# Kernel tuning notes

Hardware: AMD Instinct MI355X
Metric: run time of the kernel (lower is better)

Reference implementation:

```python
import jax, jax.numpy as jnp
import numpy as np

B, S, T = 1024, 512, 48


def setup_inputs() -> dict:
    key = jax.random.key(0)
    k1, k2, k3, k4, k5 = jax.random.split(key, 5)
    feats = jax.random.normal(k1, (B, S, T), dtype=jnp.float32)
    tags = jax.random.randint(k2, (B, S), 0, T)
    mask = jnp.ones((B, S), dtype=bool)
    transitions = jax.random.normal(k3, (T, T), dtype=jnp.float32)
    start_transitions = jax.random.normal(k4, (T,), dtype=jnp.float32)
    stop_transitions = jax.random.normal(k5, (T,), dtype=jnp.float32)
    return dict(feats=feats, tags=tags, mask=mask, transitions=transitions,
                start_transitions=start_transitions, stop_transitions=stop_transitions)


def _crf_nll(feats, transitions, start_transitions, stop_transitions, tags, mask):
    # ----- forward algorithm (log partition) -----
    fv0 = start_transitions + feats[:, 0]                      # (B, T)

    def step(fv, xs):
        feat_t, mask_t = xs                                    # (B, T), (B,)
        # transitions[next, cur]: fv over cur axis (last)
        nxt = jax.nn.logsumexp(fv[:, None, :] + transitions[None, :, :]
                               + feat_t[:, :, None], axis=-1)  # (B, T)
        fv = jnp.where(mask_t[:, None], nxt, fv)
        return fv, None

    feats_t = jnp.swapaxes(feats, 0, 1)                        # (S, B, T)
    fv, _ = jax.lax.scan(step, fv0, (feats_t[1:], mask.T[1:]))
    log_z = jax.nn.logsumexp(fv + stop_transitions, axis=-1)   # (B,)

    # ----- gold path score -----
    emit = jnp.take_along_axis(feats, tags[..., None], axis=2)[..., 0]   # (B, S)
    trans = transitions[tags[:, 1:], tags[:, :-1]]                       # (B, S-1)
    gold = emit[:, 0] + start_transitions[tags[:, 0]]
    gold = gold + jnp.sum(jnp.where(mask[:, 1:], trans + emit[:, 1:], 0.0), axis=1)
    last_idx = mask.astype(jnp.int32).sum(axis=1) - 1                    # (B,)
    last_tag = jnp.take_along_axis(tags, last_idx[:, None], axis=1)[:, 0]
    gold = gold + stop_transitions[last_tag]

    return jnp.mean(log_z - gold)


def reference(feats, tags, mask, transitions, start_transitions, stop_transitions):
    return _crf_nll(feats, transitions, start_transitions, stop_transitions, tags, mask)
```

## Files before the change

### kernel.cpp

```cpp
#include <hip/hip_runtime.h>
#include <hip/hip_bf16.h>
#include <math.h>

#define BB 1024
#define SS 512
#define MID 256
#define TT 48
#define BPW 16
#define FWB 16
#define BWB 16

typedef __attribute__((ext_vector_type(8))) short short8;
typedef __attribute__((ext_vector_type(4))) float f32x4;
typedef __attribute__((ext_vector_type(4))) unsigned u32x4;
typedef __attribute__((ext_vector_type(2))) unsigned u32x2;

__device__ __forceinline__ unsigned short f2bf_u(float x) {
    return __builtin_bit_cast(unsigned short, __float2bfloat16(x));
}
__device__ __forceinline__ unsigned pk_bf16(float lo, float hi) {
    return (unsigned)f2bf_u(lo) | ((unsigned)f2bf_u(hi) << 16);
}
__device__ __forceinline__ short f2bf(float x) { return (short)f2bf_u(x); }

template<int CTRL>
__device__ __forceinline__ float dpp_f(float v) {
    int r = __builtin_amdgcn_update_dpp(0, __builtin_bit_cast(int, v),
                                        CTRL, 0xF, 0xF, true);
    return __builtin_bit_cast(float, r);
}
__device__ __forceinline__ float waveSum(float v) {
    v += dpp_f<0x111>(v);
    v += dpp_f<0x112>(v);
    v += dpp_f<0x114>(v);
    v += dpp_f<0x118>(v);
    v += dpp_f<0x142>(v);
    v += dpp_f<0x143>(v);
    return __builtin_bit_cast(float,
        __builtin_amdgcn_readlane(__builtin_bit_cast(int, v), 63));
}

__global__ __launch_bounds__(256, 1) void crf_main(
    const float* __restrict__ feats, const int* __restrict__ tags,
    const float* __restrict__ trans, const float* __restrict__ startT,
    const float* __restrict__ stopT,
    float* __restrict__ qf, float* __restrict__ cf,
    float* __restrict__ qb, float* __restrict__ cb,
    float* __restrict__ gold)
{
    const int wv = threadIdx.x >> 6;
    const int lane = threadIdx.x & 63;

    if (blockIdx.x < FWB + BWB) {
        const bool isF = blockIdx.x < FWB;
        __shared__ unsigned Qb_[4][16][28];
        __shared__ int ptab[4][16];
        const int c = lane & 15;
        const int g = lane >> 4;
        const int bi = isF ? blockIdx.x : (blockIdx.x - FWB);
        const int b0 = (bi * 4 + wv) * BPW;
        const float* fb = feats + (size_t)(b0 + c) * SS * TT;
        unsigned (*Q)[28] = Qb_[wv];

        int pic;
        {
            if (lane < 16) ptab[wv][lane] = lane;
            const short one = f2bf(1.0f);
            short8 PA, PB;
            #pragma unroll
            for (int j = 0; j < 8; j++) {
                PA[j] = (g == 0) ? one : (short)0;
                PB[j] = f2bf((float)c);
            }
            f32x4 z = {0.f, 0.f, 0.f, 0.f};
            f32x4 PD = __builtin_amdgcn_mfma_f32_16x16x32_bf16(PA, PB, z, 0, 0, 0);
            int piv = (int)(PD[0] * 0.125f + 0.5f);
            piv = piv < 0 ? 0 : (piv > 15 ? 15 : piv);
            if (g == 0) ptab[wv][piv] = c;
            pic = ptab[wv][c];
            pic = pic < 0 ? 0 : (pic > 15 ? 15 : pic);
        }

        short8 Afr[3][2];
        #pragma unroll
        for (int r = 0; r < 3; r++)
            #pragma unroll
            for (int s = 0; s < 2; s++) {
                short8 v;
                #pragma unroll
                for (int j = 0; j < 8; j++) {
                    int k = 8 * g + j + 32 * s;
                    int row = 16 * r + c;
                    float e = (k < TT)
                        ? __expf(isF ? trans[row * TT + k] : trans[k * TT + row])
                        : 0.0f;
                    v[j] = f2bf(e);
                }
                Afr[r][s] = v;
            }

        f32x4 prods[3];
        float c_acc = 0.0f;
        float pend_is = 1.0f, pend_lg = 0.0f;
        f32x4 rA[3], rB[3], Ecur[3];

        #define PUBLISH_READ() do {                                          \
            _Pragma("unroll")                                                \
            for (int r = 0; r < 3; r++) {                                    \
                u32x2 w = { pk_bf16(prods[r][0], prods[r][1]),               \
                            pk_bf16(prods[r][2], prods[r][3]) };             \
                *(u32x2*)(&Q[c][8 * r + 2 * g]) = w;                         \
            }                                                                \
            const unsigned* src = &Q[pic][0];                                \
            B0 = __builtin_bit_cast(short8, *(const u32x4*)(src + 4 * g));   \
            if (g < 2)                                                       \
                B1 = __builtin_bit_cast(short8, *(const u32x4*)(src + 16 + 4 * g)); \
            else { u32x4 zz = {0u,0u,0u,0u}; B1 = __builtin_bit_cast(short8, zz); } \
        } while (0)

        #define MEASURE() do {                                               \
            float mx = 0.0f;                                                 \
            _Pragma("unroll")                                                \
            for (int r = 0; r < 3; r++)                                      \
                _Pragma("unroll")                                            \
                for (int j = 0; j < 4; j++) {                                \
                    prods[r][j] = fminf(prods[r][j], 1e30f);                 \
                    mx = fmaxf(mx, prods[r][j]);                             \
                }                                                            \
            mx = fmaxf(mx, __shfl_xor(mx, 16));                              \
            mx = fmaxf(mx, __shfl_xor(mx, 32));                              \
            mx = fminf(fmaxf(mx, 1e-30f), 3e37f);                            \
            pend_is = __builtin_amdgcn_rcpf(mx);                             \
            pend_lg = __logf(mx);                                            \
        } while (0)

        #define FOLD() do {                                                  \
            c_acc += pend_lg;                                                \
            _Pragma("unroll")                                                \
            for (int r = 0; r < 3; r++) Ecur[r] *= pend_is;                  \
        } while (0)

        short8 B0, B1;

        if (isF) {
            {
                f32x4 fv[3];
                #pragma unroll
                for (int r = 0; r < 3; r++) {
                    f32x4 st = *(const f32x4*)(startT + 16 * r + 4 * g);
                    f32x4 f0 = *(const f32x4*)(fb + 16 * r + 4 * g);
                    fv[r] = st + f0;
                }
                float mx = fv[0][0];
                #pragma unroll
                for (int r = 0; r < 3; r++)
                    #pragma unroll
                    for (int j = 0; j < 4; j++) mx = fmaxf(mx, fv[r][j]);
                mx = fmaxf(mx, __shfl_xor(mx, 16));
                mx = fmaxf(mx, __shfl_xor(mx, 32));
                c_acc = mx;
                #pragma unroll
                for (int r = 0; r < 3; r++)
                    #pragma unroll
                    for (int j = 0; j < 4; j++)
                        prods[r][j] = __expf(fv[r][j] - mx);
            }
            PUBLISH_READ();
            #pragma unroll
            for (int r = 0; r < 3; r++) {
                f32x4 r1 = *(const f32x4*)(fb + (size_t)1 * TT + 16 * r + 4 * g);
                rA[r] = *(const f32x4*)(fb + (size_t)2 * TT + 16 * r + 4 * g);
                rB[r] = *(const f32x4*)(fb + (size_t)3 * TT + 16 * r + 4 * g);
                f32x4 e;
                #pragma unroll
                for (int j = 0; j < 4; j++) e[j] = __expf(r1[j]);
                Ecur[r] = e;
            }

            #pragma unroll 4
            for (int t = 1; t <= MID; t++) {
                int tl = (t + 3 <= MID) ? t + 3 : MID;
                f32x4 rN[3];
                #pragma unroll
                for (int r = 0; r < 3; r++)
                    rN[r] = *(const f32x4*)(fb + (size_t)tl * TT + 16 * r + 4 * g);

                f32x4 D[3];
                #pragma unroll
                for (int r = 0; r < 3; r++) {
                    f32x4 z = {0.f, 0.f, 0.f, 0.f};
                    z = __builtin_amdgcn_mfma_f32_16x16x32_bf16(Afr[r][0], B0, z, 0, 0, 0);
                    z = __builtin_amdgcn_mfma_f32_16x16x32_bf16(Afr[r][1], B1, z, 0, 0, 0);
                    D[r] = z;
                }
                if ((t & 3) == 1) FOLD();
                #pragma unroll
                for (int r = 0; r < 3; r++) prods[r] = D[r] * Ecur[r];
                if ((t & 3) == 0) MEASURE();
                PUBLISH_READ();
                #pragma unroll
                for (int r = 0; r < 3; r++) {
                    f32x4 e;
                    #pragma unroll
                    for (int j = 0; j < 4; j++) e[j] = __expf(rA[r][j]);
                    Ecur[r] = e;
                    rA[r] = rB[r];
                    rB[r] = rN[r];
                }
            }
            #pragma unroll
            for (int r = 0; r < 3; r++)
                *(f32x4*)(qf + (size_t)(b0 + c) * TT + 16 * r + 4 * g) = prods[r];
            if (g == 0) cf[b0 + c] = c_acc;
        } else {
            #pragma unroll
            for (int r = 0; r < 3; r++) {
                f32x4 sp = *(const f32x4*)(stopT + 16 * r + 4 * g);
                #pragma unroll
                for (int j = 0; j < 4; j++) prods[r][j] = __expf(sp[j]);
            }
            #pragma unroll
            for (int r = 0; r < 3; r++) {
                f32x4 r1 = *(const f32x4*)(fb + (size_t)(SS - 1) * TT + 16 * r + 4 * g);
                rA[r] = *(const f32x4*)(fb + (size_t)(SS - 2) * TT + 16 * r + 4 * g);
                rB[r] = *(const f32x4*)(fb + (size_t)(SS - 3) * TT + 16 * r + 4 * g);
                f32x4 e;
                #pragma unroll
                for (int j = 0; j < 4; j++) e[j] = __expf(r1[j]);
                Ecur[r] = e;
            }

            #pragma unroll 4
            for (int t = SS - 1; t >= MID + 1; t--) {
                int tl = (t - 3 >= 0) ? t - 3 : 0;
                f32x4 rN[3];
                #pragma unroll
                for (int r = 0; r < 3; r++)
                    rN[r] = *(const f32x4*)(fb + (size_t)tl * TT + 16 * r + 4 * g);

                if ((t & 3) == 3) FOLD();
                #pragma unroll
                for (int r = 0; r < 3; r++) prods[r] = prods[r] * Ecur[r];
                PUBLISH_READ();
                f32x4 D[3];
                #pragma unroll
                for (int r = 0; r < 3; r++) {
                    f32x4 z = {0.f, 0.f, 0.f, 0.f};
                    z = __builtin_amdgcn_mfma_f32_16x16x32_bf16(Afr[r][0], B0, z, 0, 0, 0);
                    z = __builtin_amdgcn_mfma_f32_16x16x32_bf16(Afr[r][1], B1, z, 0, 0, 0);
                    D[r] = z;
                }
                #pragma unroll
                for (int r = 0; r < 3; r++) prods[r] = D[r];
                if ((t & 3) == 0) MEASURE();
                #pragma unroll
                for (int r = 0; r < 3; r++) {
                    f32x4 e;
                    #pragma unroll
                    for (int j = 0; j < 4; j++) e[j] = __expf(rA[r][j]);
                    Ecur[r] = e;
                    rA[r] = rB[r];
                    rB[r] = rN[r];
                }
            }
            #pragma unroll
            for (int r = 0; r < 3; r++)
                *(f32x4*)(qb + (size_t)(b0 + c) * TT + 16 * r + 4 * g) = prods[r];
            if (g == 0) cb[b0 + c] = c_acc;
        }
        #undef PUBLISH_READ
        #undef MEASURE
        #undef FOLD
    } else {
        const int b = (blockIdx.x - FWB - BWB) * 4 + wv;
        const int* tg = tags + b * SS;
        const float* fbg = feats + (size_t)b * SS * TT;
        float acc = 0.0f;
        for (int t = lane; t < SS; t += 64) {
            int cur = tg[t];
            if (t == 0) {
                acc += fbg[cur] + startT[cur];
            } else {
                int prev = tg[t - 1];
                acc += fbg[t * TT + cur] + trans[cur * TT + prev];
            }
        }
        float tot = waveSum(acc);
        if (lane == 0) gold[b] = tot + stopT[tg[SS - 1]];
    }
}

__global__ __launch_bounds__(256) void crf_final(
    const float* __restrict__ qf, const float* __restrict__ cf,
    const float* __restrict__ qb, const float* __restrict__ cb,
    const float* __restrict__ gold, float* __restrict__ out)
{
    __shared__ double sh[256];
    int t = threadIdx.x;
    double s = 0.0;
    for (int b = t * 4; b < t * 4 + 4; b++) {
        float acc = 0.0f;
        for (int j = 0; j < TT; j++)
            acc += qf[(size_t)b * TT + j] * qb[(size_t)b * TT + j];
        acc = fminf(fmaxf(acc, 1e-35f), 3e37f);
        float lz = cf[b] + cb[b] + __logf(acc);
        s += (double)lz - (double)gold[b];
    }
    sh[t] = s;
    __syncthreads();
    for (int ofs = 128; ofs > 0; ofs >>= 1) {
        if (t < ofs) sh[t] += sh[t + ofs];
        __syncthreads();
    }
    if (t == 0) out[0] = (float)(sh[0] / (double)BB);
}

extern "C" void kernel_launch(void* const* d_in, const int* in_sizes, int n_in,
                              void* d_out, int out_size, void* d_ws, size_t ws_size,
                              hipStream_t stream)
{
    const float* feats  = (const float*)d_in[0];
    const int*   tags   = (const int*)d_in[1];
    const float* trans  = (const float*)d_in[3];
    const float* startT = (const float*)d_in[4];
    const float* stopT  = (const float*)d_in[5];

    float* gold = (float*)d_ws;
    float* qf   = gold + BB;
    float* cf   = qf + BB * TT;
    float* qb   = cf + BB;
    float* cb   = qb + BB * TT;

    crf_main<<<FWB + BWB + 256, 256, 0, stream>>>(
        feats, tags, trans, startT, stopT, qf, cf, qb, cb, gold);
    crf_final<<<1, 256, 0, stream>>>(qf, cf, qb, cb, gold, (float*)d_out);
}
```

Before: 123.0 us.

## Precompute exp(feats) as bf16 in a parallel prepass before the sequential CRF scan

Adds a bandwidth-parallel prepass kernel that exponentiates all emission scores and stores them as bf16 in workspace, computing the gold path scores in the same launch. The sequential forward/backward kernel then loads half as many bytes per step and only bit-unpacks them, with no exp on the recurrence path. The sequential kernel now uses 8 waves per 512-thread block and prefetches four steps ahead instead of three. The cost is an extra full pass over feats plus a large workspace write, and emissions lose precision when rounded to bf16. A fallback path without the prepass is kept for when the workspace is too small.

```diff
diff --git a/kernel.cpp b/kernel.cpp
--- a/kernel.cpp
+++ b/kernel.cpp
@@ -1,14 +1,13 @@
 #include <hip/hip_runtime.h>
 #include <hip/hip_bf16.h>
 #include <math.h>
+#include <type_traits>
 
 #define BB 1024
 #define SS 512
 #define MID 256
 #define TT 48
-#define BPW 16
-#define FWB 16
-#define BWB 16
+#define CONVB 1024
 
 typedef __attribute__((ext_vector_type(8))) short short8;
 typedef __attribute__((ext_vector_type(4))) float f32x4;
@@ -22,6 +21,15 @@
     return (unsigned)f2bf_u(lo) | ((unsigned)f2bf_u(hi) << 16);
 }
 __device__ __forceinline__ short f2bf(float x) { return (short)f2bf_u(x); }
+
+__device__ __forceinline__ f32x4 unpk4(u32x2 w) {
+    f32x4 e;
+    e[0] = __builtin_bit_cast(float, w[0] << 16);
+    e[1] = __builtin_bit_cast(float, w[0] & 0xffff0000u);
+    e[2] = __builtin_bit_cast(float, w[1] << 16);
+    e[3] = __builtin_bit_cast(float, w[1] & 0xffff0000u);
+    return e;
+}
 
 template<int CTRL>
 __device__ __forceinline__ float dpp_f(float v) {
@@ -40,254 +48,294 @@
         __builtin_amdgcn_readlane(__builtin_bit_cast(int, v), 63));
 }
 
-__global__ __launch_bounds__(256, 1) void crf_main(
-    const float* __restrict__ feats, const int* __restrict__ tags,
-    const float* __restrict__ trans, const float* __restrict__ startT,
-    const float* __restrict__ stopT,
+__device__ __forceinline__ void gold_wave(
+    int b, int lane, const float* feats, const int* tags, const float* trans,
+    const float* startT, const float* stopT, float* gold)
+{
+    const int* tg = tags + b * SS;
+    const float* fbg = feats + (size_t)b * SS * TT;
+    float acc = 0.0f;
+    for (int t = lane; t < SS; t += 64) {
+        int cur = tg[t];
+        if (t == 0) {
+            acc += fbg[cur] + startT[cur];
+        } else {
+            int prev = tg[t - 1];
+            acc += fbg[t * TT + cur] + trans[cur * TT + prev];
+        }
+    }
+    float tot = waveSum(acc);
+    if (lane == 0) gold[b] = tot + stopT[tg[SS - 1]];
+}
+
+__global__ __launch_bounds__(256) void crf_prepass(
+    const float* __restrict__ feats, unsigned short* __restrict__ G,
+    const int* __restrict__ tags, const float* __restrict__ trans,
+    const float* __restrict__ startT, const float* __restrict__ stopT,
+    float* __restrict__ gold)
+{
+    if (blockIdx.x < CONVB) {
+        const size_t NB4 = (size_t)BB * SS * TT / 4;
+        const float4* src = (const float4*)feats;
+        ushort4* dst = (ushort4*)G;
+        for (size_t i = (size_t)blockIdx.x * 256 + threadIdx.x; i < NB4;
+             i += (size_t)CONVB * 256) {
+            float4 v = src[i];
+            ushort4 o;
+            o.x = f2bf_u(__expf(v.x));
+            o.y = f2bf_u(__expf(v.y));
+            o.z = f2bf_u(__expf(v.z));
+            o.w = f2bf_u(__expf(v.w));
+            dst[i] = o;
+        }
+    } else {
+        const int wv = threadIdx.x >> 6;
+        const int lane = threadIdx.x & 63;
+        gold_wave((blockIdx.x - CONVB) * 4 + wv, lane,
+                  feats, tags, trans, startT, stopT, gold);
+    }
+}
+
+template<bool PRE>
+__global__ __launch_bounds__(512, 2) void crf_seq(
+    const float* __restrict__ feats, const unsigned short* __restrict__ G,
+    const int* __restrict__ tags, const float* __restrict__ trans,
+    const float* __restrict__ startT, const float* __restrict__ stopT,
     float* __restrict__ qf, float* __restrict__ cf,
     float* __restrict__ qb, float* __restrict__ cb,
     float* __restrict__ gold)
 {
-    const int wv = threadIdx.x >> 6;
+    const int w = threadIdx.x >> 6;
     const int lane = threadIdx.x & 63;
 
-    if (blockIdx.x < FWB + BWB) {
-        const bool isF = blockIdx.x < FWB;
-        __shared__ unsigned Qb_[4][16][28];
-        __shared__ int ptab[4][16];
-        const int c = lane & 15;
-        const int g = lane >> 4;
-        const int bi = isF ? blockIdx.x : (blockIdx.x - FWB);
-        const int b0 = (bi * 4 + wv) * BPW;
-        const float* fb = feats + (size_t)(b0 + c) * SS * TT;
-        unsigned (*Q)[28] = Qb_[wv];
-
-        int pic;
+    if (blockIdx.x >= 16) {
+        gold_wave((blockIdx.x - 16) * 8 + w, lane,
+                  feats, tags, trans, startT, stopT, gold);
+        return;
+    }
+
+    const bool isF = blockIdx.x < 8;
+    __shared__ unsigned Q_[8][16][28];
+    __shared__ int ptab[8][16];
+    const int c = lane & 15;
+    const int g = lane >> 4;
+    const int bi = (isF ? blockIdx.x : blockIdx.x - 8) * 8 + w;
+    const int b0 = bi * 16;
+    const float* fb = feats + (size_t)(b0 + c) * SS * TT;
+    const unsigned short* gb = G + (size_t)(b0 + c) * SS * TT;
+    unsigned (*Q)[28] = Q_[w];
+
+    int pic;
+    {
+        if (lane < 16) ptab[w][lane] = lane;
+        const short one = f2bf(1.0f);
+        short8 PA, PB;
+        #pragma unroll
+        for (int j = 0; j < 8; j++) {
+            PA[j] = (g == 0) ? one : (short)0;
+            PB[j] = f2bf((float)c);
+        }
+        f32x4 z = {0.f, 0.f, 0.f, 0.f};
+        f32x4 PD = __builtin_amdgcn_mfma_f32_16x16x32_bf16(PA, PB, z, 0, 0, 0);
+        int piv = (int)(PD[0] * 0.125f + 0.5f);
+        piv = piv < 0 ? 0 : (piv > 15 ? 15 : piv);
+        if (g == 0) ptab[w][piv] = c;
+        pic = ptab[w][c];
+        pic = pic < 0 ? 0 : (pic > 15 ? 15 : pic);
+    }
+
+    short8 Afr[3][2];
+    #pragma unroll
+    for (int r = 0; r < 3; r++)
+        #pragma unroll
+        for (int s = 0; s < 2; s++) {
+            short8 v;
+            #pragma unroll
+            for (int j = 0; j < 8; j++) {
+                int k = 8 * g + j + 32 * s;
+                int row = 16 * r + c;
+                float e = (k < TT)
+                    ? __expf(isF ? trans[row * TT + k] : trans[k * TT + row])
+                    : 0.0f;
+                v[j] = f2bf(e);
+            }
+            Afr[r][s] = v;
+        }
+
+    auto LD = [&](int t, int r) {
+        if constexpr (PRE)
+            return *(const u32x2*)(gb + (size_t)t * TT + 16 * r + 4 * g);
+        else
+            return *(const f32x4*)(fb + (size_t)t * TT + 16 * r + 4 * g);
+    };
+    auto PROM = [&](auto v) -> f32x4 {
+        if constexpr (PRE) {
+            return unpk4(v);
+        } else {
+            f32x4 e;
+            #pragma unroll
+            for (int j = 0; j < 4; j++) e[j] = __expf(v[j]);
+            return e;
+        }
+    };
+    using LT = decltype(LD(0, 0));
+
+    f32x4 prods[3];
+    float c_acc = 0.0f;
+    float pend_is = 1.0f, pend_lg = 0.0f;
+    LT rA[3], rB[3], rC[3];
+    f32x4 Ecur[3];
+    short8 B0, B1;
+
+    #define PUBLISH_READ() do {                                          \
+        _Pragma("unroll")                                                \
+        for (int r = 0; r < 3; r++) {                                    \
+            u32x2 wd = { pk_bf16(prods[r][0], prods[r][1]),              \
+                         pk_bf16(prods[r][2], prods[r][3]) };            \
+            *(u32x2*)(&Q[c][8 * r + 2 * g]) = wd;                        \
+        }                                                                \
+        const unsigned* src = &Q[pic][0];                                \
+        B0 = __builtin_bit_cast(short8, *(const u32x4*)(src + 4 * g));   \
+        if (g < 2)                                                       \
+            B1 = __builtin_bit_cast(short8, *(const u32x4*)(src + 16 + 4 * g)); \
+        else { u32x4 zz = {0u,0u,0u,0u}; B1 = __builtin_bit_cast(short8, zz); } \
+    } while (0)
+
+    #define MEASURE() do {                                               \
+        float mx = 0.0f;                                                 \
+        _Pragma("unroll")                                                \
+        for (int r = 0; r < 3; r++)                                      \
+            _Pragma("unroll")                                            \
+            for (int j = 0; j < 4; j++) {                                \
+                prods[r][j] = fminf(prods[r][j], 1e30f);                 \
+                mx = fmaxf(mx, prods[r][j]);                             \
+            }                                                            \
+        mx = fmaxf(mx, __shfl_xor(mx, 16));                              \
+        mx = fmaxf(mx, __shfl_xor(mx, 32));                              \
+        mx = fminf(fmaxf(mx, 1e-30f), 3e37f);                            \
+        pend_is = __builtin_amdgcn_rcpf(mx);                             \
+        pend_lg = __logf(mx);                                            \
+    } while (0)
+
+    #define FOLD() do {                                                  \
+        c_acc += pend_lg;                                                \
+        _Pragma("unroll")                                                \
+        for (int r = 0; r < 3; r++) Ecur[r] *= pend_is;                  \
+    } while (0)
+
+    if (isF) {
         {
-            if (lane < 16) ptab[wv][lane] = lane;
-            const short one = f2bf(1.0f);
-            short8 PA, PB;
-            #pragma unroll
-            for (int j = 0; j < 8; j++) {
-                PA[j] = (g == 0) ? one : (short)0;
-                PB[j] = f2bf((float)c);
-            }
-            f32x4 z = {0.f, 0.f, 0.f, 0.f};
-            f32x4 PD = __builtin_amdgcn_mfma_f32_16x16x32_bf16(PA, PB, z, 0, 0, 0);
-            int piv = (int)(PD[0] * 0.125f + 0.5f);
-            piv = piv < 0 ? 0 : (piv > 15 ? 15 : piv);
-            if (g == 0) ptab[wv][piv] = c;
-            pic = ptab[wv][c];
-            pic = pic < 0 ? 0 : (pic > 15 ? 15 : pic);
-        }
-
-        short8 Afr[3][2];
+            f32x4 fv[3];
+            #pragma unroll
+            for (int r = 0; r < 3; r++) {
+                f32x4 st = *(const f32x4*)(startT + 16 * r + 4 * g);
+                f32x4 f0 = *(const f32x4*)(fb + 16 * r + 4 * g);
+                fv[r] = st + f0;
+            }
+            float mx = fv[0][0];
+            #pragma unroll
+            for (int r = 0; r < 3; r++)
+                #pragma unroll
+                for (int j = 0; j < 4; j++) mx = fmaxf(mx, fv[r][j]);
+            mx = fmaxf(mx, __shfl_xor(mx, 16));
+            mx = fmaxf(mx, __shfl_xor(mx, 32));
+            c_acc = mx;
+            #pragma unroll
+            for (int r = 0; r < 3; r++)
+                #pragma unroll
+                for (int j = 0; j < 4; j++)
+                    prods[r][j] = __expf(fv[r][j] - mx);
+        }
+        PUBLISH_READ();
+        #pragma unroll
+        for (int r = 0; r < 3; r++) {
+            Ecur[r] = PROM(LD(1, r));
+            rA[r] = LD(2, r);
+            rB[r] = LD(3, r);
+            rC[r] = LD(4, r);
+        }
+
+        #pragma unroll 4
+        for (int t = 1; t <= MID; t++) {
+            int tl = (t + 4 <= MID) ? t + 4 : MID;
+            LT rN[3];
+            #pragma unroll
+            for (int r = 0; r < 3; r++) rN[r] = LD(tl, r);
+
+            f32x4 D[3];
+            #pragma unroll
+            for (int r = 0; r < 3; r++) {
+                f32x4 z = {0.f, 0.f, 0.f, 0.f};
+                z = __builtin_amdgcn_mfma_f32_16x16x32_bf16(Afr[r][0], B0, z, 0, 0, 0);
+                z = __builtin_amdgcn_mfma_f32_16x16x32_bf16(Afr[r][1], B1, z, 0, 0, 0);
+                D[r] = z;
+            }
+            if ((t & 3) == 1) FOLD();
+            #pragma unroll
+            for (int r = 0; r < 3; r++) prods[r] = D[r] * Ecur[r];
+            if ((t & 3) == 0) MEASURE();
+            PUBLISH_READ();
+            #pragma unroll
+            for (int r = 0; r < 3; r++) {
+                Ecur[r] = PROM(rA[r]);
+                rA[r] = rB[r]; rB[r] = rC[r]; rC[r] = rN[r];
+            }
+        }
         #pragma unroll
         for (int r = 0; r < 3; r++)
-            #pragma unroll
-            for (int s = 0; s < 2; s++) {
-                short8 v;
-                #pragma unroll
-                for (int j = 0; j < 8; j++) {
-                    int k = 8 * g + j + 32 * s;
-                    int row = 16 * r + c;
-                    float e = (k < TT)
-                        ? __expf(isF ? trans[row * TT + k] : trans[k * TT + row])
-                        : 0.0f;
-                    v[j] = f2bf(e);
-                }
-                Afr[r][s] = v;
-            }
-
-        f32x4 prods[3];
-        float c_acc = 0.0f;
-        float pend_is = 1.0f, pend_lg = 0.0f;
-        f32x4 rA[3], rB[3], Ecur[3];
-
-        #define PUBLISH_READ() do {                                          \
-            _Pragma("unroll")                                                \
-            for (int r = 0; r < 3; r++) {                                    \
-                u32x2 w = { pk_bf16(prods[r][0], prods[r][1]),               \
-                            pk_bf16(prods[r][2], prods[r][3]) };             \
-                *(u32x2*)(&Q[c][8 * r + 2 * g]) = w;                         \
-            }                                                                \
-            const unsigned* src = &Q[pic][0];                                \
-            B0 = __builtin_bit_cast(short8, *(const u32x4*)(src + 4 * g));   \
-            if (g < 2)                                                       \
-                B1 = __builtin_bit_cast(short8, *(const u32x4*)(src + 16 + 4 * g)); \
-            else { u32x4 zz = {0u,0u,0u,0u}; B1 = __builtin_bit_cast(short8, zz); } \
-        } while (0)
-
-        #define MEASURE() do {                                               \
-            float mx = 0.0f;                                                 \
-            _Pragma("unroll")                                                \
-            for (int r = 0; r < 3; r++)                                      \
-                _Pragma("unroll")                                            \
-                for (int j = 0; j < 4; j++) {                                \
-                    prods[r][j] = fminf(prods[r][j], 1e30f);                 \
-                    mx = fmaxf(mx, prods[r][j]);                             \
-                }                                                            \
-            mx = fmaxf(mx, __shfl_xor(mx, 16));                              \
-            mx = fmaxf(mx, __shfl_xor(mx, 32));                              \
-            mx = fminf(fmaxf(mx, 1e-30f), 3e37f);                            \
-            pend_is = __builtin_amdgcn_rcpf(mx);                             \
-            pend_lg = __logf(mx);                                            \
-        } while (0)
-
-        #define FOLD() do {                                                  \
-            c_acc += pend_lg;                                                \
-            _Pragma("unroll")                                                \
-            for (int r = 0; r < 3; r++) Ecur[r] *= pend_is;                  \
-        } while (0)
-
-        short8 B0, B1;
-
-        if (isF) {
-            {
-                f32x4 fv[3];
-                #pragma unroll
-                for (int r = 0; r < 3; r++) {
-                    f32x4 st = *(const f32x4*)(startT + 16 * r + 4 * g);
-                    f32x4 f0 = *(const f32x4*)(fb + 16 * r + 4 * g);
-                    fv[r] = st + f0;
-                }
-                float mx = fv[0][0];
-                #pragma unroll
-                for (int r = 0; r < 3; r++)
-                    #pragma unroll
-                    for (int j = 0; j < 4; j++) mx = fmaxf(mx, fv[r][j]);
-                mx = fmaxf(mx, __shfl_xor(mx, 16));
-                mx = fmaxf(mx, __shfl_xor(mx, 32));
-                c_acc = mx;
-                #pragma unroll
-                for (int r = 0; r < 3; r++)
-                    #pragma unroll
-                    for (int j = 0; j < 4; j++)
-                        prods[r][j] = __expf(fv[r][j] - mx);
-            }
+            *(f32x4*)(qf + (size_t)(b0 + c) * TT + 16 * r + 4 * g) = prods[r];
+        if (g == 0) cf[b0 + c] = c_acc;
+    } else {
+        #pragma unroll
+        for (int r = 0; r < 3; r++) {
+            f32x4 sp = *(const f32x4*)(stopT + 16 * r + 4 * g);
+            #pragma unroll
+            for (int j = 0; j < 4; j++) prods[r][j] = __expf(sp[j]);
+        }
+        #pragma unroll
+        for (int r = 0; r < 3; r++) {
+            Ecur[r] = PROM(LD(SS - 1, r));
+            rA[r] = LD(SS - 2, r);
+            rB[r] = LD(SS - 3, r);
+            rC[r] = LD(SS - 4, r);
+        }
+
+        #pragma unroll 4
+        for (int t = SS - 1; t >= MID + 1; t--) {
+            int tl = (t - 4 >= 0) ? t - 4 : 0;
+            LT rN[3];
+            #pragma unroll
+            for (int r = 0; r < 3; r++) rN[r] = LD(tl, r);
+
+            if ((t & 3) == 3) FOLD();
+            #pragma unroll
+            for (int r = 0; r < 3; r++) prods[r] = prods[r] * Ecur[r];
             PUBLISH_READ();
-            #pragma unroll
-            for (int r = 0; r < 3; r++) {
-                f32x4 r1 = *(const f32x4*)(fb + (size_t)1 * TT + 16 * r + 4 * g);
-                rA[r] = *(const f32x4*)(fb + (size_t)2 * TT + 16 * r + 4 * g);
-                rB[r] = *(const f32x4*)(fb + (size_t)3 * TT + 16 * r + 4 * g);
-                f32x4 e;
-                #pragma unroll
-                for (int j = 0; j < 4; j++) e[j] = __expf(r1[j]);
-                Ecur[r] = e;
-            }
-
-            #pragma unroll 4
-            for (int t = 1; t <= MID; t++) {
-                int tl = (t + 3 <= MID) ? t + 3 : MID;
-                f32x4 rN[3];
-                #pragma unroll
-                for (int r = 0; r < 3; r++)
-                    rN[r] = *(const f32x4*)(fb + (size_t)tl * TT + 16 * r + 4 * g);
-
-                f32x4 D[3];
-                #pragma unroll
-                for (int r = 0; r < 3; r++) {
-                    f32x4 z = {0.f, 0.f, 0.f, 0.f};
-                    z = __builtin_amdgcn_mfma_f32_16x16x32_bf16(Afr[r][0], B0, z, 0, 0, 0);
-                    z = __builtin_amdgcn_mfma_f32_16x16x32_bf16(Afr[r][1], B1, z, 0, 0, 0);
-                    D[r] = z;
-                }
-                if ((t & 3) == 1) FOLD();
-                #pragma unroll
-                for (int r = 0; r < 3; r++) prods[r] = D[r] * Ecur[r];
-                if ((t & 3) == 0) MEASURE();
-                PUBLISH_READ();
-                #pragma unroll
-                for (int r = 0; r < 3; r++) {
-                    f32x4 e;
-                    #pragma unroll
-                    for (int j = 0; j < 4; j++) e[j] = __expf(rA[r][j]);
-                    Ecur[r] = e;
-                    rA[r] = rB[r];
-                    rB[r] = rN[r];
-                }
-            }
-            #pragma unroll
-            for (int r = 0; r < 3; r++)
-                *(f32x4*)(qf + (size_t)(b0 + c) * TT + 16 * r + 4 * g) = prods[r];
-            if (g == 0) cf[b0 + c] = c_acc;
-        } else {
-            #pragma unroll
-            for (int r = 0; r < 3; r++) {
-                f32x4 sp = *(const f32x4*)(stopT + 16 * r + 4 * g);
-                #pragma unroll
-                for (int j = 0; j < 4; j++) prods[r][j] = __expf(sp[j]);
-            }
-            #pragma unroll
-            for (int r = 0; r < 3; r++) {
-                f32x4 r1 = *(const f32x4*)(fb + (size_t)(SS - 1) * TT + 16 * r + 4 * g);
-                rA[r] = *(const f32x4*)(fb + (size_t)(SS - 2) * TT + 16 * r + 4 * g);
-                rB[r] = *(const f32x4*)(fb + (size_t)(SS - 3) * TT + 16 * r + 4 * g);
-                f32x4 e;
-                #pragma unroll
-                for (int j = 0; j < 4; j++) e[j] = __expf(r1[j]);
-                Ecur[r] = e;
-            }
-
-            #pragma unroll 4
-            for (int t = SS - 1; t >= MID + 1; t--) {
-                int tl = (t - 3 >= 0) ? t - 3 : 0;
-                f32x4 rN[3];
-                #pragma unroll
-                for (int r = 0; r < 3; r++)
-                    rN[r] = *(const f32x4*)(fb + (size_t)tl * TT + 16 * r + 4 * g);
-
-                if ((t & 3) == 3) FOLD();
-                #pragma unroll
-                for (int r = 0; r < 3; r++) prods[r] = prods[r] * Ecur[r];
-                PUBLISH_READ();
-                f32x4 D[3];
-                #pragma unroll
-                for (int r = 0; r < 3; r++) {
-                    f32x4 z = {0.f, 0.f, 0.f, 0.f};
-                    z = __builtin_amdgcn_mfma_f32_16x16x32_bf16(Afr[r][0], B0, z, 0, 0, 0);
-                    z = __builtin_amdgcn_mfma_f32_16x16x32_bf16(Afr[r][1], B1, z, 0, 0, 0);
-                    D[r] = z;
-                }
-                #pragma unroll
-                for (int r = 0; r < 3; r++) prods[r] = D[r];
-                if ((t & 3) == 0) MEASURE();
-                #pragma unroll
-                for (int r = 0; r < 3; r++) {
-                    f32x4 e;
-                    #pragma unroll
-                    for (int j = 0; j < 4; j++) e[j] = __expf(rA[r][j]);
-                    Ecur[r] = e;
-                    rA[r] = rB[r];
-                    rB[r] = rN[r];
-                }
-            }
-            #pragma unroll
-            for (int r = 0; r < 3; r++)
-                *(f32x4*)(qb + (size_t)(b0 + c) * TT + 16 * r + 4 * g) = prods[r];
-            if (g == 0) cb[b0 + c] = c_acc;
-        }
-        #undef PUBLISH_READ
-        #undef MEASURE
-        #undef FOLD
-    } else {
-        const int b = (blockIdx.x - FWB - BWB) * 4 + wv;
-        const int* tg = tags + b * SS;
-        const float* fbg = feats + (size_t)b * SS * TT;
-        float acc = 0.0f;
-        for (int t = lane; t < SS; t += 64) {
-            int cur = tg[t];
-            if (t == 0) {
-                acc += fbg[cur] + startT[cur];
-            } else {
-                int prev = tg[t - 1];
-                acc += fbg[t * TT + cur] + trans[cur * TT + prev];
-            }
-        }
-        float tot = waveSum(acc);
-        if (lane == 0) gold[b] = tot + stopT[tg[SS - 1]];
-    }
+            f32x4 D[3];
+            #pragma unroll
+            for (int r = 0; r < 3; r++) {
+                f32x4 z = {0.f, 0.f, 0.f, 0.f};
+                z = __builtin_amdgcn_mfma_f32_16x16x32_bf16(Afr[r][0], B0, z, 0, 0, 0);
+                z = __builtin_amdgcn_mfma_f32_16x16x32_bf16(Afr[r][1], B1, z, 0, 0, 0);
+                D[r] = z;
+            }
+            #pragma unroll
+            for (int r = 0; r < 3; r++) prods[r] = D[r];
+            if ((t & 3) == 0) MEASURE();
+            #pragma unroll
+            for (int r = 0; r < 3; r++) {
+                Ecur[r] = PROM(rA[r]);
+                rA[r] = rB[r]; rB[r] = rC[r]; rC[r] = rN[r];
+            }
+        }
+        #pragma unroll
+        for (int r = 0; r < 3; r++)
+            *(f32x4*)(qb + (size_t)(b0 + c) * TT + 16 * r + 4 * g) = prods[r];
+        if (g == 0) cb[b0 + c] = c_acc;
+    }
+    #undef PUBLISH_READ
+    #undef MEASURE
+    #undef FOLD
 }
 
 __global__ __launch_bounds__(256) void crf_final(
@@ -325,13 +373,26 @@
     const float* startT = (const float*)d_in[4];
     const float* stopT  = (const float*)d_in[5];
 
-    float* gold = (float*)d_ws;
-    float* qf   = gold + BB;
-    float* cf   = qf + BB * TT;
-    float* qb   = cf + BB;
-    float* cb   = qb + BB * TT;
-
-    crf_main<<<FWB + BWB + 256, 256, 0, stream>>>(
-        feats, tags, trans, startT, stopT, qf, cf, qb, cb, gold);
+    const size_t GBYTES = (size_t)BB * SS * TT * 2;
+    const size_t TAILF  = (size_t)BB * (1 + TT + 1 + TT + 1);
+    const bool pre = ws_size >= GBYTES + TAILF * 4 + 64;
+
+    char* p = (char*)d_ws;
+    unsigned short* G = (unsigned short*)p;
+    float* gold = (float*)(p + (pre ? GBYTES : 0));
+    float* qf = gold + BB;
+    float* cf = qf + BB * TT;
+    float* qb = cf + BB;
+    float* cb = qb + BB * TT;
+
+    if (pre) {
+        crf_prepass<<<CONVB + 256, 256, 0, stream>>>(
+            feats, G, tags, trans, startT, stopT, gold);
+        crf_seq<true><<<16, 512, 0, stream>>>(
+            feats, G, tags, trans, startT, stopT, qf, cf, qb, cb, gold);
+    } else {
+        crf_seq<false><<<16 + 128, 512, 0, stream>>>(
+            feats, G, tags, trans, startT, stopT, qf, cf, qb, cb, gold);
+    }
     crf_final<<<1, 256, 0, stream>>>(qf, cf, qb, cb, gold, (float*)d_out);
 }
```

New measurement: 230.2 us. +87.2%, slower.
